# Performance work log

Hardware: AMD Instinct MI355X
Metric: run time of the kernel (lower is better)

The kernel has to match this reference:

```python
import jax, jax.numpy as jnp
import numpy as np

N, E, D, F = 8192, 262144, 256, 512  # nodes, edges, hidden_dim, ffn hidden
M = 256  # performer num_random_features (default)


def _ln(x, g, b, eps=1e-5):
    mu = jnp.mean(x, axis=-1, keepdims=True)
    var = jnp.mean((x - mu) ** 2, axis=-1, keepdims=True)
    return (x - mu) * jax.lax.rsqrt(var + eps) * g + b


def setup_inputs() -> dict:
    key = jax.random.key(0)
    ks = jax.random.split(key, 16)
    s = 1.0 / np.sqrt(D)
    return {
        "h": jax.random.normal(ks[0], (N, D), dtype=jnp.float32),
        "edge_index": jax.random.randint(ks[1], (2, E), 0, N, dtype=jnp.int32),
        "W_gcn": jax.random.normal(ks[2], (D, D), dtype=jnp.float32) * s,
        "b_gcn": jnp.zeros((D,), jnp.float32),
        "Wq": jax.random.normal(ks[3], (D, D), dtype=jnp.float32) * s,
        "bq": jnp.zeros((D,), jnp.float32),
        "Wk": jax.random.normal(ks[4], (D, D), dtype=jnp.float32) * s,
        "bk": jnp.zeros((D,), jnp.float32),
        "Wv": jax.random.normal(ks[5], (D, D), dtype=jnp.float32) * s,
        "bv": jnp.zeros((D,), jnp.float32),
        "Wo": jax.random.normal(ks[6], (D, D), dtype=jnp.float32) * s,
        "bo": jnp.zeros((D,), jnp.float32),
        "RF": jax.random.normal(ks[7], (M, D), dtype=jnp.float32) * s,  # random feature projection
        "g1": jnp.ones((D,), jnp.float32), "be1": jnp.zeros((D,), jnp.float32),
        "g2": jnp.ones((D,), jnp.float32), "be2": jnp.zeros((D,), jnp.float32),
        "g3": jnp.ones((D,), jnp.float32), "be3": jnp.zeros((D,), jnp.float32),
        "W1": jax.random.normal(ks[8], (D, F), dtype=jnp.float32) * s,
        "b1": jnp.zeros((F,), jnp.float32),
        "W2": jax.random.normal(ks[9], (F, D), dtype=jnp.float32) * (1.0 / np.sqrt(F)),
        "b2": jnp.zeros((D,), jnp.float32),
    }


def _gps_forward(h, edge_index, W_gcn, b_gcn, Wq, bq, Wk, bk, Wv, bv, Wo, bo, RF,
                 g1, be1, g2, be2, g3, be3, W1, b1, W2, b2):
    n = h.shape[0]
    # ---- local GCNConv (add self loops, symmetric norm) ----
    loops = jnp.arange(n, dtype=edge_index.dtype)
    src = jnp.concatenate([edge_index[0], loops])
    dst = jnp.concatenate([edge_index[1], loops])
    deg = jax.ops.segment_sum(jnp.ones_like(src, dtype=h.dtype), dst, num_segments=n)
    dinv = jnp.where(deg > 0, jax.lax.rsqrt(jnp.maximum(deg, 1e-12)), 0.0)
    coef = dinv[src] * dinv[dst]  # [E+N]
    xw = h @ W_gcn  # [N, D]
    h_local = jax.ops.segment_sum(xw[src] * coef[:, None], dst, num_segments=n) + b_gcn
    h1 = _ln(h + h_local, g1, be1)  # dropout p applied in train only; eval here
    # ---- global Performer attention (as written: dense NxN in feature space) ----
    q = h1 @ Wq + bq
    k = h1 @ Wk + bk
    v = h1 @ Wv + bv
    qf = q @ RF.T  # [N, M]
    kf = k @ RF.T  # [N, M]
    scores = (qf @ kf.T) / jnp.sqrt(jnp.asarray(h.shape[-1], h.dtype))  # [N, N]
    attw = jax.nn.softmax(scores, axis=-1)
    h_global = (attw @ v) @ Wo + bo
    h2 = _ln(h1 + h_global, g2, be2)
    # ---- FFN ----
    h_ffn = jnp.maximum(h2 @ W1 + b1, 0.0) @ W2 + b2
    return _ln(h2 + h_ffn, g3, be3)


def reference(h, edge_index, W_gcn, b_gcn, Wq, bq, Wk, bk, Wv, bv, Wo, bo, RF,
              g1, be1, g2, be2, g3, be3, W1, b1, W2, b2):
    return _gps_forward(h, edge_index, W_gcn, b_gcn, Wq, bq, Wk, bk, Wv, bv, Wo, bo, RF,
                        g1, be1, g2, be2, g3, be3, W1, b1, W2, b2)
```

## Files before the change

### kernel.cpp

```cpp
#include <hip/hip_runtime.h>
#include <hip/hip_bf16.h>

#define NN 8192
#define EE 262144
#define DD 256
#define FF 512
#define MM 256

typedef __attribute__((ext_vector_type(8))) short short8v;
typedef __attribute__((ext_vector_type(16))) float float16v;

__device__ __forceinline__ ushort f2bf(float x) {
  union { float f; unsigned u; } c; c.f = x;
  unsigned r = (c.u + 0x7FFF + ((c.u >> 16) & 1)) >> 16;
  return (ushort)r;
}
__device__ __forceinline__ float b2f(ushort u) {
  union { unsigned u; float f; } c; c.u = ((unsigned)u) << 16;
  return c.f;
}
__device__ __forceinline__ void async_copy16(void* lds, const void* g) {
  __builtin_amdgcn_global_load_lds(
      (const __attribute__((address_space(1))) void*)g,
      (__attribute__((address_space(3))) void*)lds, 16, 0, 0);
}

__global__ __launch_bounds__(1024) void scan_kernel(const int* __restrict__ degi,
                                                    int* __restrict__ csr_off,
                                                    float* __restrict__ dinv) {
  __shared__ int part[1024];
  int tid = threadIdx.x;
  int base = tid * 8;
  int loc[8], dv[8]; int s = 0;
#pragma unroll
  for (int i = 0; i < 8; ++i) { int d = degi[base + i]; dv[i] = d; loc[i] = s; s += d; }
  part[tid] = s;
  __syncthreads();
  for (int off = 1; off < 1024; off <<= 1) {
    int v = (tid >= off) ? part[tid - off] : 0;
    __syncthreads();
    part[tid] += v;
    __syncthreads();
  }
  int pre = (tid == 0) ? 0 : part[tid - 1];
#pragma unroll
  for (int i = 0; i < 8; ++i) {
    csr_off[base + i] = pre + loc[i];
    dinv[base + i] = rsqrtf((float)(dv[i] + 1));
  }
  if (tid == 1023) csr_off[NN] = part[1023];
}

__global__ void fill_kernel(const int* __restrict__ ei, const int* __restrict__ csr_off,
                            int* __restrict__ cursor, int* __restrict__ csr_src) {
  int i = blockIdx.x * blockDim.x + threadIdx.x;
  if (i < EE) {
    int d = ei[EE + i];
    int pos = csr_off[d] + atomicAdd(&cursor[d], 1);
    csr_src[pos] = ei[i];
  }
}

#define QSCALE 0.090168441f
#define P1B 10753
__global__ __launch_bounds__(256) void prep_kernel(
    const float* __restrict__ h, const float* __restrict__ W_gcn,
    const float* __restrict__ Wv, const float* __restrict__ Wo,
    const float* __restrict__ W1, const float* __restrict__ W2,
    const float* __restrict__ bv,
    const float* __restrict__ Wq, const float* __restrict__ Wk,
    const float* __restrict__ bq, const float* __restrict__ bk,
    const float* __restrict__ RF, const int* __restrict__ ei,
    ushort* __restrict__ hb, ushort* __restrict__ WgcnT, ushort* __restrict__ Wcat,
    ushort* __restrict__ WoT, ushort* __restrict__ W1T, ushort* __restrict__ W2T,
    ushort* __restrict__ RFb, ushort* __restrict__ Wqkb,
    float* __restrict__ bcat, int* __restrict__ degi)
{
  if (blockIdx.x < P1B) {
    int i = blockIdx.x * 256 + threadIdx.x;
    const int R0 = NN * DD;
    const int R1 = R0 + DD * DD;
    const int R2 = R1 + DD * DD;
    const int R3 = R2 + DD * DD;
    const int R4 = R3 + DD * FF;
    const int R5 = R4 + FF * DD;
    const int R6 = R5 + DD;
    const int R7 = R6 + DD * DD;
    const int R8 = R7 + DD * DD;
    const int R9 = R8 + DD * DD;
    if (i < R0) {
      hb[i] = f2bf(h[i]);
    } else if (i < R1) {
      int j = i - R0; int n = j >> 8, k = j & 255;
      WgcnT[(n << 8) | k] = f2bf(W_gcn[k * DD + n]);
    } else if (i < R2) {
      int j = i - R1; int n = j >> 8, k = j & 255;
      Wcat[((512 + n) << 8) | k] = f2bf(Wv[k * DD + n]);
    } else if (i < R3) {
      int j = i - R2; int n = j >> 8, k = j & 255;
      WoT[(n << 8) | k] = f2bf(Wo[k * DD + n]);
    } else if (i < R4) {
      int j = i - R3; int n = j >> 8, k = j & 255;
      W1T[(n << 8) | k] = f2bf(W1[k * FF + n]);
    } else if (i < R5) {
      int j = i - R4; int n = j >> 9, k = j & 511;
      W2T[n * FF + k] = f2bf(W2[k * DD + n]);
    } else if (i < R6) {
      bcat[512 + (i - R5)] = bv[i - R5];
    } else if (i < R7) {
      int j = i - R6;
      RFb[j] = f2bf(RF[j]);
    } else if (i < R8) {
      int j = i - R7;
      Wqkb[j] = f2bf(Wq[j] * QSCALE);
    } else if (i < R9) {
      int j = i - R8;
      Wqkb[DD * DD + j] = f2bf(Wk[j]);
    }
  } else if (blockIdx.x < P1B + 2) {
    const int b = blockIdx.x - P1B;
    const int m = threadIdx.x;
    const float* bvec = (b == 0) ? bq : bk;
    const float alpha = (b == 0) ? QSCALE : 1.0f;
    float s = 0.0f;
    for (int j = 0; j < DD; ++j) s = fmaf(bvec[j], RF[m * DD + j], s);
    bcat[(b == 0 ? 0 : 256) + m] = s * alpha;
  } else {
    int i = (blockIdx.x - P1B - 2) * 256 + threadIdx.x;
    if (i < EE) atomicAdd(&degi[ei[EE + i]], 1);
  }
}

template<int OMODE, bool RELU>
__global__ __launch_bounds__(512) void gemm_bf16_kernel(
    const ushort* __restrict__ A, const ushort* __restrict__ BT,
    const float* __restrict__ bias, void* __restrict__ Cv,
    void* __restrict__ Cv2, void* __restrict__ Cv3, void* __restrict__ Cv4,
    int M, int N, int K)
{
  __shared__ ushort As[2][4096];
  __shared__ ushort Bs[2][4096];
  const int tid = threadIdx.x;
  const int c32 = tid & 31, hi = (tid >> 5) & 1;
  const int wv = tid >> 6;
  const int q = wv & 3, ks = wv >> 2;
  const int qm = (q >> 1) << 5, qn = (q & 1) << 5;

  const ushort* pA = A;
  const ushort* pBT = BT;
  int m0 = blockIdx.y * 64;
  const int n0 = blockIdx.x * 64;
  bool xw_path = true;
  if (OMODE == 6) {
    if (blockIdx.y < 128) {
      if (blockIdx.x >= 4) return;
    } else {
      xw_path = false;
      pA = (const ushort*)Cv2;
      pBT = (const ushort*)Cv3;
      m0 = (blockIdx.y - 128) * 64;
    }
  }

  const int sr = tid >> 3, spsl = tid & 7;
  const int ssl = spsl ^ ((sr >> 2) & 7);
  const ushort* Asrc = pA + (size_t)(m0 + sr) * K + (ssl << 3);
  const ushort* Bsrc = pBT + (size_t)(n0 + sr) * K + (ssl << 3);

  const int ra = qm + c32, rb = qn + c32;
  const int ga = (ra >> 2) & 7, gb = (rb >> 2) & 7;

  float16v acc = (float16v)(0.0f);

#define GS(b, k0) { \
    async_copy16(&As[b][tid << 3], Asrc + (k0)); \
    async_copy16(&Bs[b][tid << 3], Bsrc + (k0)); }

  GS(0, 0)
  const int nk = K >> 6;
  for (int kt = 0; kt < nk; ++kt) {
    asm volatile("s_waitcnt vmcnt(0)" ::: "memory");
    __syncthreads();
    if (kt + 1 < nk) GS((kt + 1) & 1, (kt + 1) << 6)
    const ushort* as_ = As[kt & 1];
    const ushort* bs_ = Bs[kt & 1];
    __builtin_amdgcn_s_setprio(1);
#pragma unroll
    for (int k2 = 0; k2 < 2; ++k2) {
      const int k16 = (ks << 1) + k2;
      const int sl = (k16 << 1) + hi;
      short8v af = *(const short8v*)&as_[(ra << 6) + ((sl ^ ga) << 3)];
      short8v bf = *(const short8v*)&bs_[(rb << 6) + ((sl ^ gb) << 3)];
      acc = __builtin_amdgcn_mfma_f32_32x32x16_bf16(af, bf, acc, 0, 0, 0);
    }
    __builtin_amdgcn_s_setprio(0);
  }
#undef GS

  __syncthreads();
  float* red = (float*)&As[0][0];
  if (ks == 1) {
#pragma unroll
    for (int r = 0; r < 16; ++r) {
      const int crow = (r & 3) + ((r >> 2) << 3) + (hi << 2);
      red[(q << 10) + (crow << 5) + c32] = acc[r];
    }
  }
  __syncthreads();
  if (ks == 0) {
    const int col = n0 + qn + c32;
    const float bv = bias ? bias[col] : 0.0f;
    if (OMODE == 3 && col >= 512) {
#pragma unroll
      for (int g = 0; g < 4; ++g) {
        float v0 = acc[g * 4 + 0] + red[(q << 10) + (((0) + (g << 3) + (hi << 2)) << 5) + c32] + bv;
        float v1 = acc[g * 4 + 1] + red[(q << 10) + (((1) + (g << 3) + (hi << 2)) << 5) + c32] + bv;
        float v2 = acc[g * 4 + 2] + red[(q << 10) + (((2) + (g << 3) + (hi << 2)) << 5) + c32] + bv;
        float v3 = acc[g * 4 + 3] + red[(q << 10) + (((3) + (g << 3) + (hi << 2)) << 5) + c32] + bv;
        ushort4 o; o.x = f2bf(v0); o.y = f2bf(v1); o.z = f2bf(v2); o.w = f2bf(v3);
        *(ushort4*)&((ushort*)Cv3)[(size_t)(col - 512) * NN + m0 + qm + (g << 3) + (hi << 2)] = o;
      }
    } else {
#pragma unroll
      for (int r = 0; r < 16; ++r) {
        const int crow = (r & 3) + ((r >> 2) << 3) + (hi << 2);
        const int m = m0 + qm + crow;
        float v = acc[r] + red[(q << 10) + (crow << 5) + c32] + bv;
        if (RELU) v = fmaxf(v, 0.0f);
        if (OMODE == 4) {
          ((ushort*)Cv)[(size_t)m * N + col] = f2bf(v);
        } else if (OMODE == 6) {
          if (xw_path) {
            ((ushort*)Cv)[(size_t)m * 256 + col] = f2bf(v);
          } else {
            ushort* W = (ushort*)Cv4;
            if (col < 256) W[(size_t)m * 256 + col] = f2bf(v);
            else W[(size_t)(256 + m) * 256 + (col - 256)] = f2bf(v);
          }
        } else {
          if (col < 256) {
            ((ushort*)Cv)[(size_t)m * 256 + col] = f2bf(v);
          } else {
            const int c2 = (col - 256) ^ ((m & 7) << 3) ^ (((m >> 3) & 3) << 6);
            ((ushort*)Cv2)[(size_t)m * 256 + c2] = f2bf(v);
          }
        }
      }
    }
  }
}

__global__ __launch_bounds__(256) void gcn_gather_ln_kernel(
    const ushort* __restrict__ xwb, const float* __restrict__ h,
    const float* __restrict__ dinv, const int* __restrict__ csr_off,
    const int* __restrict__ csr_src, const float* __restrict__ b_gcn,
    const float* __restrict__ g1, const float* __restrict__ be1,
    ushort* __restrict__ h1b)
{
  const int node = blockIdx.x * 4 + (threadIdx.x >> 6);
  const int t = threadIdx.x & 63;
  const int c4 = t << 2;
  const float di = dinv[node];
  const int e0 = csr_off[node], e1 = csr_off[node + 1];
  float acc[4] = {0.f, 0.f, 0.f, 0.f};
  for (int e = e0; e < e1; ++e) {
    int s = csr_src[e];
    float ds = dinv[s];
    ushort4 xv = *(const ushort4*)&xwb[(size_t)s * DD + c4];
    acc[0] = fmaf(b2f(xv.x), ds, acc[0]);
    acc[1] = fmaf(b2f(xv.y), ds, acc[1]);
    acc[2] = fmaf(b2f(xv.z), ds, acc[2]);
    acc[3] = fmaf(b2f(xv.w), ds, acc[3]);
  }
  ushort4 sv = *(const ushort4*)&xwb[(size_t)node * DD + c4];
  float4 hv = *(const float4*)&h[(size_t)node * DD + c4];
  float4 bg = *(const float4*)&b_gcn[c4];
  const float dii = di * di;
  float y[4];
  y[0] = fmaf(acc[0], di, b2f(sv.x) * dii) + bg.x + hv.x;
  y[1] = fmaf(acc[1], di, b2f(sv.y) * dii) + bg.y + hv.y;
  y[2] = fmaf(acc[2], di, b2f(sv.z) * dii) + bg.z + hv.z;
  y[3] = fmaf(acc[3], di, b2f(sv.w) * dii) + bg.w + hv.w;
  float s1 = (y[0] + y[1]) + (y[2] + y[3]);
  float s2 = (y[0]*y[0] + y[1]*y[1]) + (y[2]*y[2] + y[3]*y[3]);
#pragma unroll
  for (int m = 1; m <= 32; m <<= 1) { s1 += __shfl_xor(s1, m); s2 += __shfl_xor(s2, m); }
  float mu = s1 * (1.0f / 256.0f);
  float var = s2 * (1.0f / 256.0f) - mu * mu;
  float inv = rsqrtf(fmaxf(var, 0.0f) + 1e-5f);
  float4 g4 = *(const float4*)&g1[c4];
  float4 b4 = *(const float4*)&be1[c4];
  float v0 = (y[0] - mu) * inv * g4.x + b4.x;
  float v1 = (y[1] - mu) * inv * g4.y + b4.y;
  float v2 = (y[2] - mu) * inv * g4.z + b4.z;
  float v3 = (y[3] - mu) * inv * g4.w + b4.w;
  ushort4 ob; ob.x = f2bf(v0); ob.y = f2bf(v1); ob.z = f2bf(v2); ob.w = f2bf(v3);
  *(ushort4*)&h1b[(node << 8) + c4] = ob;
}

__global__ __launch_bounds__(256, 2) void flash_mfma_kernel(
    const ushort* __restrict__ qb, const ushort* __restrict__ kb,
    const ushort* __restrict__ vbT, ushort* __restrict__ opb,
    float* __restrict__ ml, int ksn, int kchunk)
{
  __shared__ ushort Kbuf[2][8192];
  __shared__ ushort Vbuf[2][8192];

  const int tid = threadIdx.x;
  const int l = tid & 63, wv = tid >> 6;
  const int c32 = l & 31, hi = l >> 5;
  const int qt = blockIdx.x / ksn, ks = blockIdx.x % ksn;
  const int q0 = qt * 128;
  const int kbase = ks * kchunk;

  const int vrow = tid >> 2;
  const ushort* kptr = kb + (size_t)(kbase + (tid >> 5)) * 256 + ((tid & 31) << 3);
  const ushort* vptr = vbT + (size_t)vrow * NN + kbase + (((tid & 3) ^ ((vrow >> 3) & 3)) << 3);

#define FSTAGE(b) { \
    _Pragma("unroll") \
    for (int c = 0; c < 4; ++c) { \
      async_copy16(&Kbuf[b][((c << 8) + tid) << 3], kptr + (size_t)c * (8 * 256)); \
      async_copy16(&Vbuf[b][((c << 8) + tid) << 3], vptr + (size_t)c * (64 * NN)); \
    } }

  FSTAGE(0)

  short8v qfr[16];
  {
    const ushort* qrow = qb + (size_t)(q0 + wv * 32 + c32) * 256 + (hi << 3);
#pragma unroll
    for (int kk = 0; kk < 16; ++kk)
      qfr[kk] = *(const short8v*)(qrow + (kk << 4));
  }

  float16v acc[8];
#pragma unroll
  for (int dt = 0; dt < 8; ++dt) acc[dt] = (float16v)(0.0f);
  float lsum = 0.f;

  const int ksw = ((c32 & 7) << 3) | (((c32 >> 3) & 3) << 6);
  const int vsw = (c32 >> 3) & 3;
  const int voff0 = (hi ^ vsw) << 3;
  const int voff1 = ((2 + hi) ^ vsw) << 3;

  const int nit = kchunk >> 5;
  for (int it = 0; it < nit; ++it) {
    asm volatile("s_waitcnt vmcnt(0)" ::: "memory");
    __syncthreads();
    if (it + 1 < nit) {
      kptr += 32 * 256;
      vptr += 32;
      FSTAGE((it + 1) & 1)
    }
    const ushort* Kp = Kbuf[it & 1];
    const ushort* Vp = Vbuf[it & 1];

    float16v s = (float16v)(0.0f);
    __builtin_amdgcn_s_setprio(1);
#pragma unroll
    for (int kk = 0; kk < 16; ++kk) {
      short8v kf = *(const short8v*)&Kp[(c32 << 8) + (((kk << 4) + (hi << 3)) ^ ksw)];
      s = __builtin_amdgcn_mfma_f32_32x32x16_bf16(kf, qfr[kk], s, 0, 0, 0);
    }
    __builtin_amdgcn_s_setprio(0);

    float p[16];
#pragma unroll
    for (int r = 0; r < 16; ++r) p[r] = exp2f(s[r]);
    {
      float t0 = (p[0] + p[1]) + (p[2] + p[3]);
      float t1 = (p[4] + p[5]) + (p[6] + p[7]);
      float t2 = (p[8] + p[9]) + (p[10] + p[11]);
      float t3 = (p[12] + p[13]) + (p[14] + p[15]);
      lsum += (t0 + t1) + (t2 + t3);
    }
    unsigned u0, u1, u2, u3, u4, u5, u6, u7;
    asm("v_cvt_pk_bf16_f32 %0, %1, %2" : "=v"(u0) : "v"(p[0]),  "v"(p[1]));
    asm("v_cvt_pk_bf16_f32 %0, %1, %2" : "=v"(u1) : "v"(p[2]),  "v"(p[3]));
    asm("v_cvt_pk_bf16_f32 %0, %1, %2" : "=v"(u2) : "v"(p[4]),  "v"(p[5]));
    asm("v_cvt_pk_bf16_f32 %0, %1, %2" : "=v"(u3) : "v"(p[6]),  "v"(p[7]));
    asm("v_cvt_pk_bf16_f32 %0, %1, %2" : "=v"(u4) : "v"(p[8]),  "v"(p[9]));
    asm("v_cvt_pk_bf16_f32 %0, %1, %2" : "=v"(u5) : "v"(p[10]), "v"(p[11]));
    asm("v_cvt_pk_bf16_f32 %0, %1, %2" : "=v"(u6) : "v"(p[12]), "v"(p[13]));
    asm("v_cvt_pk_bf16_f32 %0, %1, %2" : "=v"(u7) : "v"(p[14]), "v"(p[15]));
    asm volatile("v_permlane32_swap_b32 %0, %1" : "+v"(u0), "+v"(u2));
    asm volatile("v_permlane32_swap_b32 %0, %1" : "+v"(u1), "+v"(u3));
    asm volatile("v_permlane32_swap_b32 %0, %1" : "+v"(u4), "+v"(u6));
    asm volatile("v_permlane32_swap_b32 %0, %1" : "+v"(u5), "+v"(u7));
    union { unsigned uu[4]; short8v v; } P0, P1;
    P0.uu[0] = u0; P0.uu[1] = u1; P0.uu[2] = u2; P0.uu[3] = u3;
    P1.uu[0] = u4; P1.uu[1] = u5; P1.uu[2] = u6; P1.uu[3] = u7;

    __builtin_amdgcn_s_setprio(1);
#pragma unroll
    for (int dt = 0; dt < 8; ++dt) {
      const int drow = (dt << 5) + c32;
      short8v vf0 = *(const short8v*)&Vp[(drow << 5) + voff0];
      short8v vf1 = *(const short8v*)&Vp[(drow << 5) + voff1];
      acc[dt] = __builtin_amdgcn_mfma_f32_32x32x16_bf16(P0.v, vf0, acc[dt], 0, 0, 0);
      acc[dt] = __builtin_amdgcn_mfma_f32_32x32x16_bf16(P1.v, vf1, acc[dt], 0, 0, 0);
    }
    __builtin_amdgcn_s_setprio(0);
  }
#undef FSTAGE

  float lt = lsum + __shfl_xor(lsum, 32);
  if (hi == 0) ml[(size_t)ks * NN + q0 + wv * 32 + c32] = lt;
  ushort* op = opb + (size_t)ks * (NN * DD);
#pragma unroll
  for (int dt = 0; dt < 8; ++dt)
#pragma unroll
    for (int r = 0; r < 16; ++r) {
      const int qrow = q0 + wv * 32 + (r & 3) + ((r >> 2) << 3) + (hi << 2);
      op[(size_t)qrow * DD + (dt << 5) + c32] = f2bf(acc[dt][r]);
    }
}

__global__ __launch_bounds__(512, 4) void epilogue_kernel(
    const ushort* __restrict__ opb, const float* __restrict__ ml,
    const ushort* __restrict__ h1b,
    const ushort* __restrict__ WoT, const float* __restrict__ bo,
    const float* __restrict__ g2, const float* __restrict__ be2,
    const ushort* __restrict__ W1T, const float* __restrict__ b1,
    const ushort* __restrict__ W2T, const float* __restrict__ b2,
    const float* __restrict__ g3, const float* __restrict__ be3,
    float* __restrict__ out, int ksn)
{
  __shared__ float  yL[32 * 256];
  __shared__ ushort h2bL[32 * 256];
  __shared__ ushort tL[32 * 512];

  ushort* hgL = tL;

  const int tid = threadIdx.x;
  const int c32 = tid & 31, hi = (tid >> 5) & 1;
  const int wv = tid >> 6;
  const int lane = tid & 63;
  const int m0 = blockIdx.x * 32;
  const int n0 = wv << 5;
  const int col = n0 + c32;

  {
    const int row = tid >> 4;
    const int cseg = (tid & 15) << 4;
    const int growp = m0 + row;
    float L = 0.f;
    for (int i = 0; i < ksn; ++i) L += ml[(size_t)i * NN + growp];
    const float invl = 1.0f / L;
    float num[16];
#pragma unroll
    for (int j = 0; j < 16; ++j) num[j] = 0.f;
    for (int i = 0; i < ksn; ++i) {
      const ushort* src = opb + (size_t)i * ((size_t)NN * DD) + (size_t)growp * DD + cseg;
      short8v v0 = *(const short8v*)src;
      short8v v1 = *(const short8v*)(src + 8);
#pragma unroll
      for (int j = 0; j < 8; ++j) {
        num[j]     += b2f((ushort)v0[j]);
        num[8 + j] += b2f((ushort)v1[j]);
      }
    }
    const int swz = (row & 7) ^ (((row >> 3) & 3) << 3);
    const int sl0 = (cseg >> 3);
    union { ushort us[8]; short8v v; } o0, o1;
#pragma unroll
    for (int j = 0; j < 8; ++j) {
      o0.us[j] = f2bf(num[j] * invl);
      o1.us[j] = f2bf(num[8 + j] * invl);
    }
    *(short8v*)&hgL[(row << 8) + ((sl0 ^ swz) << 3)] = o0.v;
    *(short8v*)&hgL[(row << 8) + (((sl0 + 1) ^ swz) << 3)] = o1.v;
  }
  __syncthreads();

  float16v acc = (float16v)(0.0f);
  {
    const int aswz = (c32 & 7) ^ (((c32 >> 3) & 3) << 3);
#pragma unroll
    for (int k0 = 0; k0 < 256; k0 += 16) {
      const int sA = (k0 >> 3) + hi;
      short8v af = *(const short8v*)&hgL[(c32 << 8) + ((sA ^ aswz) << 3)];
      short8v bf = *(const short8v*)&WoT[(size_t)col * 256 + k0 + (hi << 3)];
      acc = __builtin_amdgcn_mfma_f32_32x32x16_bf16(af, bf, acc, 0, 0, 0);
    }
  }
  {
    const float bov = bo[col];
#pragma unroll
    for (int r = 0; r < 16; ++r) {
      const int row = (r & 3) + ((r >> 2) << 3) + (hi << 2);
      yL[(row << 8) + col] = acc[r] + bov + b2f(h1b[(size_t)(m0 + row) * 256 + col]);
    }
  }
  __syncthreads();
#pragma unroll
  for (int rr = 0; rr < 4; ++rr) {
    const int row = (wv << 2) + rr;
    const int c4 = lane << 2;
    float4 v = *(const float4*)&yL[(row << 8) + c4];
    float s1 = (v.x + v.y) + (v.z + v.w);
    float s2 = (v.x * v.x + v.y * v.y) + (v.z * v.z + v.w * v.w);
#pragma unroll
    for (int m = 1; m <= 32; m <<= 1) { s1 += __shfl_xor(s1, m); s2 += __shfl_xor(s2, m); }
    float mu = s1 * (1.0f / 256.0f);
    float var = s2 * (1.0f / 256.0f) - mu * mu;
    float inv = rsqrtf(fmaxf(var, 0.0f) + 1e-5f);
    float4 g4 = *(const float4*)&g2[c4];
    float4 b4 = *(const float4*)&be2[c4];
    float o0 = (v.x - mu) * inv * g4.x + b4.x;
    float o1 = (v.y - mu) * inv * g4.y + b4.y;
    float o2 = (v.z - mu) * inv * g4.z + b4.z;
    float o3 = (v.w - mu) * inv * g4.w + b4.w;
    *(float4*)&yL[(row << 8) + c4] = make_float4(o0, o1, o2, o3);
    const int psl = (c4 >> 3) ^ (row & 7);
    ushort4 ob; ob.x = f2bf(o0); ob.y = f2bf(o1); ob.z = f2bf(o2); ob.w = f2bf(o3);
    *(ushort4*)&h2bL[(row << 8) + (psl << 3) + (c4 & 7)] = ob;
  }
  __syncthreads();
  {
    float16v a1[2] = {(float16v)(0.0f), (float16v)(0.0f)};
    const int f0 = wv << 6;
#pragma unroll
    for (int k0 = 0; k0 < 256; k0 += 16) {
      const int s = (k0 >> 3) + hi;
      short8v af = *(const short8v*)&h2bL[(c32 << 8) + ((s ^ (c32 & 7)) << 3)];
#pragma unroll
      for (int nt = 0; nt < 2; ++nt) {
        short8v bf = *(const short8v*)&W1T[(size_t)(f0 + (nt << 5) + c32) * 256 + k0 + (hi << 3)];
        a1[nt] = __builtin_amdgcn_mfma_f32_32x32x16_bf16(af, bf, a1[nt], 0, 0, 0);
      }
    }
#pragma unroll
    for (int nt = 0; nt < 2; ++nt) {
      const int col1 = f0 + (nt << 5) + c32;
      const float b1v = b1[col1];
#pragma unroll
      for (int r = 0; r < 16; ++r) {
        const int row = (r & 3) + ((r >> 2) << 3) + (hi << 2);
        float v = fmaxf(a1[nt][r] + b1v, 0.0f);
        const int psl = (col1 >> 3) ^ (row & 7);
        tL[(row << 9) + (psl << 3) + (col1 & 7)] = f2bf(v);
      }
    }
  }
  __syncthreads();
  float16v a2 = (float16v)(0.0f);
#pragma unroll
  for (int k0 = 0; k0 < 512; k0 += 16) {
    const int s = (k0 >> 3) + hi;
    short8v af = *(const short8v*)&tL[(c32 << 9) + ((s ^ (c32 & 7)) << 3)];
    short8v bf = *(const short8v*)&W2T[(size_t)col * 512 + k0 + (hi << 3)];
    a2 = __builtin_amdgcn_mfma_f32_32x32x16_bf16(af, bf, a2, 0, 0, 0);
  }
  {
    const float b2v = b2[col];
#pragma unroll
    for (int r = 0; r < 16; ++r) {
      const int row = (r & 3) + ((r >> 2) << 3) + (hi << 2);
      a2[r] += b2v + yL[(row << 8) + col];
    }
  }
  __syncthreads();
  {
    float* y2L = (float*)tL;
#pragma unroll
    for (int r = 0; r < 16; ++r) {
      const int row = (r & 3) + ((r >> 2) << 3) + (hi << 2);
      y2L[(row << 8) + col] = a2[r];
    }
  }
  __syncthreads();
  {
    const float* y2L = (const float*)tL;
#pragma unroll
    for (int rr = 0; rr < 4; ++rr) {
      const int row = (wv << 2) + rr;
      const int c4 = lane << 2;
      float4 v = *(const float4*)&y2L[(row << 8) + c4];
      float s1 = (v.x + v.y) + (v.z + v.w);
      float s2 = (v.x * v.x + v.y * v.y) + (v.z * v.z + v.w * v.w);
#pragma unroll
      for (int m = 1; m <= 32; m <<= 1) { s1 += __shfl_xor(s1, m); s2 += __shfl_xor(s2, m); }
      float mu = s1 * (1.0f / 256.0f);
      float var = s2 * (1.0f / 256.0f) - mu * mu;
      float inv = rsqrtf(fmaxf(var, 0.0f) + 1e-5f);
      float4 g4 = *(const float4*)&g3[c4];
      float4 b4 = *(const float4*)&be3[c4];
      float4 o;
      o.x = (v.x - mu) * inv * g4.x + b4.x;
      o.y = (v.y - mu) * inv * g4.y + b4.y;
      o.z = (v.z - mu) * inv * g4.z + b4.z;
      o.w = (v.w - mu) * inv * g4.w + b4.w;
      *(float4*)&out[(size_t)(m0 + row) * 256 + c4] = o;
    }
  }
}

extern "C" void kernel_launch(void* const* d_in, const int* in_sizes, int n_in,
                              void* d_out, int out_size, void* d_ws, size_t ws_size,
                              hipStream_t stream) {
  (void)in_sizes; (void)n_in; (void)out_size;
  const float* h     = (const float*)d_in[0];
  const int*   ei    = (const int*)  d_in[1];
  const float* W_gcn = (const float*)d_in[2];
  const float* b_gcn = (const float*)d_in[3];
  const float* Wq    = (const float*)d_in[4];
  const float* bq    = (const float*)d_in[5];
  const float* Wk    = (const float*)d_in[6];
  const float* bk    = (const float*)d_in[7];
  const float* Wv    = (const float*)d_in[8];
  const float* bv    = (const float*)d_in[9];
  const float* Wo    = (const float*)d_in[10];
  const float* bo    = (const float*)d_in[11];
  const float* RF    = (const float*)d_in[12];
  const float* g1    = (const float*)d_in[13];
  const float* be1   = (const float*)d_in[14];
  const float* g2    = (const float*)d_in[15];
  const float* be2   = (const float*)d_in[16];
  const float* g3    = (const float*)d_in[17];
  const float* be3   = (const float*)d_in[18];
  const float* W1    = (const float*)d_in[19];
  const float* b1    = (const float*)d_in[20];
  const float* W2    = (const float*)d_in[21];
  const float* b2    = (const float*)d_in[22];
  float* out = (float*)d_out;

  const size_t M2 = (size_t)NN * DD;
  const int ksn = (ws_size >= (size_t)64 * 1024 * 1024) ? 8 : 4;
  const int kchunk = NN / ksn;

  char* base = (char*)d_ws;
  ushort* hbX  = (ushort*)base; base += M2 * 2;
  ushort* h1bX = (ushort*)base; base += M2 * 2;
  ushort* qb   = (ushort*)base; base += M2 * 2;
  ushort* kb   = (ushort*)base; base += M2 * 2;
  ushort* vbT  = (ushort*)base; base += M2 * 2;
  ushort* opb  = (ushort*)base;
  float*  R    = (float*)opb;   base += (size_t)ksn * M2 * 2;
  float*  mlf  = (float*)base;  base += (size_t)8 * NN * 4;
  ushort* WgcnT = (ushort*)base; base += DD * DD * 2;
  ushort* Wcat  = (ushort*)base; base += (size_t)768 * DD * 2;
  ushort* WoT   = (ushort*)base; base += DD * DD * 2;
  ushort* W1T   = (ushort*)base; base += FF * DD * 2;
  ushort* W2T   = (ushort*)base; base += DD * FF * 2;
  ushort* RFb   = (ushort*)base; base += DD * DD * 2;
  ushort* Wqkb  = (ushort*)base; base += (size_t)2 * DD * DD * 2;
  float*  bcat  = (float*)base;  base += 768 * 4;
  float*  dinv  = (float*)base;  base += NN * 4;
  int* degi    = (int*)base; base += NN * 4;
  int* cursor  = (int*)base; base += NN * 4;
  int* csr_off = (int*)base; base += (NN + 4) * 4;
  int* csr_src = (int*)base; base += EE * 4;

  ushort* xwb = (ushort*)R;

  hipMemsetAsync(degi, 0, (size_t)2 * NN * sizeof(int), stream);

  prep_kernel<<<P1B + 2 + 1024, 256, 0, stream>>>(
      h, W_gcn, Wv, Wo, W1, W2, bv, Wq, Wk, bq, bk, RF, ei,
      hbX, WgcnT, Wcat, WoT, W1T, W2T, RFb, Wqkb, bcat, degi);

  gemm_bf16_kernel<6, false><<<dim3(8, 132), 512, 0, stream>>>(
      hbX, WgcnT, nullptr, xwb, RFb, Wqkb, Wcat, NN, DD, DD);

  scan_kernel<<<1, 1024, 0, stream>>>(degi, csr_off, dinv);
  fill_kernel<<<EE / 256, 256, 0, stream>>>(ei, csr_off, cursor, csr_src);

  gcn_gather_ln_kernel<<<NN / 4, 256, 0, stream>>>(xwb, h, dinv, csr_off, csr_src, b_gcn, g1, be1, h1bX);
  gemm_bf16_kernel<3, false><<<dim3(768 / 64, NN / 64), 512, 0, stream>>>(
      h1bX, Wcat, bcat, qb, kb, vbT, nullptr, NN, 768, DD);
  flash_mfma_kernel<<<(NN / 128) * ksn, 256, 0, stream>>>(qb, kb, vbT, opb, mlf, ksn, kchunk);
  epilogue_kernel<<<NN / 32, 512, 0, stream>>>(
      opb, mlf, h1bX, WoT, bo, g2, be2, W1T, b1, W2T, b2, g3, be3, out, ksn);
}
```

Measured before the change: 212.6 us.

## Load full-K A tile once and loop over multiple N tiles per block

The bf16 GEMM kernel now loads the whole 64x256 A tile (full K=256) into LDS once with an XOR swizzle. It then iterates over several 64-wide N tiles, loading each full-K B tile in turn. This removes the K-loop double buffering and the repeated A reloads across N-tile blocks, and launches far fewer blocks for the xw/RF and QKV projections. The cost is much more LDS per block (64KB for the tiles plus 16KB for the reduction) and serialized B loads, with only a partial overlap of the next B load against the epilogue.

```diff
diff --git a/kernel.cpp b/kernel.cpp
--- a/kernel.cpp
+++ b/kernel.cpp
@@ -132,14 +132,16 @@
 }
 
 template<int OMODE, bool RELU>
-__global__ __launch_bounds__(512) void gemm_bf16_kernel(
+__global__ __launch_bounds__(512, 2) void gemm_v3_kernel(
     const ushort* __restrict__ A, const ushort* __restrict__ BT,
     const float* __restrict__ bias, void* __restrict__ Cv,
     void* __restrict__ Cv2, void* __restrict__ Cv3, void* __restrict__ Cv4,
-    int M, int N, int K)
+    int NT)
 {
-  __shared__ ushort As[2][4096];
-  __shared__ ushort Bs[2][4096];
+  __shared__ ushort As[16384];
+  __shared__ ushort Bs[16384];
+  __shared__ float  red[4096];
+
   const int tid = threadIdx.x;
   const int c32 = tid & 31, hi = (tid >> 5) & 1;
   const int wv = tid >> 6;
@@ -149,105 +151,103 @@
   const ushort* pA = A;
   const ushort* pBT = BT;
   int m0 = blockIdx.y * 64;
-  const int n0 = blockIdx.x * 64;
+  int nt = NT;
   bool xw_path = true;
   if (OMODE == 6) {
-    if (blockIdx.y < 128) {
-      if (blockIdx.x >= 4) return;
-    } else {
+    if (blockIdx.y >= 128) {
       xw_path = false;
       pA = (const ushort*)Cv2;
       pBT = (const ushort*)Cv3;
       m0 = (blockIdx.y - 128) * 64;
-    }
-  }
-
-  const int sr = tid >> 3, spsl = tid & 7;
-  const int ssl = spsl ^ ((sr >> 2) & 7);
-  const ushort* Asrc = pA + (size_t)(m0 + sr) * K + (ssl << 3);
-  const ushort* Bsrc = pBT + (size_t)(n0 + sr) * K + (ssl << 3);
+      nt = 4;
+    }
+  }
+
+#pragma unroll
+  for (int i = 0; i < 4; ++i) {
+    int c = tid + (i << 9);
+    int row = c >> 5, psl = c & 31;
+    int ssl = psl ^ (row & 31);
+    async_copy16(&As[c << 3], &pA[(size_t)(m0 + row) * 256 + (ssl << 3)]);
+  }
+
+#define GSB(n0_) { \
+    _Pragma("unroll") \
+    for (int i = 0; i < 4; ++i) { \
+      int c = tid + (i << 9); \
+      int row = c >> 5, psl = c & 31; \
+      int ssl = psl ^ (row & 31); \
+      async_copy16(&Bs[c << 3], &pBT[(size_t)((n0_) + row) * 256 + (ssl << 3)]); \
+    } }
+
+  GSB((size_t)blockIdx.x * nt * 64)
 
   const int ra = qm + c32, rb = qn + c32;
-  const int ga = (ra >> 2) & 7, gb = (rb >> 2) & 7;
-
-  float16v acc = (float16v)(0.0f);
-
-#define GS(b, k0) { \
-    async_copy16(&As[b][tid << 3], Asrc + (k0)); \
-    async_copy16(&Bs[b][tid << 3], Bsrc + (k0)); }
-
-  GS(0, 0)
-  const int nk = K >> 6;
-  for (int kt = 0; kt < nk; ++kt) {
+  for (int j = 0; j < nt; ++j) {
+    const int n0 = (blockIdx.x * nt + j) * 64;
     asm volatile("s_waitcnt vmcnt(0)" ::: "memory");
     __syncthreads();
-    if (kt + 1 < nk) GS((kt + 1) & 1, (kt + 1) << 6)
-    const ushort* as_ = As[kt & 1];
-    const ushort* bs_ = Bs[kt & 1];
+    float16v acc = (float16v)(0.0f);
     __builtin_amdgcn_s_setprio(1);
 #pragma unroll
-    for (int k2 = 0; k2 < 2; ++k2) {
-      const int k16 = (ks << 1) + k2;
-      const int sl = (k16 << 1) + hi;
-      short8v af = *(const short8v*)&as_[(ra << 6) + ((sl ^ ga) << 3)];
-      short8v bf = *(const short8v*)&bs_[(rb << 6) + ((sl ^ gb) << 3)];
+    for (int kk = 0; kk < 8; ++kk) {
+      const int sl = (((ks << 3) + kk) << 1) + hi;
+      short8v af = *(const short8v*)&As[(ra << 8) + ((sl ^ c32) << 3)];
+      short8v bf = *(const short8v*)&Bs[(rb << 8) + ((sl ^ c32) << 3)];
       acc = __builtin_amdgcn_mfma_f32_32x32x16_bf16(af, bf, acc, 0, 0, 0);
     }
     __builtin_amdgcn_s_setprio(0);
-  }
-#undef GS
-
-  __syncthreads();
-  float* red = (float*)&As[0][0];
-  if (ks == 1) {
-#pragma unroll
-    for (int r = 0; r < 16; ++r) {
-      const int crow = (r & 3) + ((r >> 2) << 3) + (hi << 2);
-      red[(q << 10) + (crow << 5) + c32] = acc[r];
-    }
-  }
-  __syncthreads();
-  if (ks == 0) {
-    const int col = n0 + qn + c32;
-    const float bv = bias ? bias[col] : 0.0f;
-    if (OMODE == 3 && col >= 512) {
-#pragma unroll
-      for (int g = 0; g < 4; ++g) {
-        float v0 = acc[g * 4 + 0] + red[(q << 10) + (((0) + (g << 3) + (hi << 2)) << 5) + c32] + bv;
-        float v1 = acc[g * 4 + 1] + red[(q << 10) + (((1) + (g << 3) + (hi << 2)) << 5) + c32] + bv;
-        float v2 = acc[g * 4 + 2] + red[(q << 10) + (((2) + (g << 3) + (hi << 2)) << 5) + c32] + bv;
-        float v3 = acc[g * 4 + 3] + red[(q << 10) + (((3) + (g << 3) + (hi << 2)) << 5) + c32] + bv;
-        ushort4 o; o.x = f2bf(v0); o.y = f2bf(v1); o.z = f2bf(v2); o.w = f2bf(v3);
-        *(ushort4*)&((ushort*)Cv3)[(size_t)(col - 512) * NN + m0 + qm + (g << 3) + (hi << 2)] = o;
-      }
-    } else {
+    __syncthreads();
+    if (j + 1 < nt) GSB((size_t)(blockIdx.x * nt + j + 1) * 64)
+    if (ks == 1) {
 #pragma unroll
       for (int r = 0; r < 16; ++r) {
         const int crow = (r & 3) + ((r >> 2) << 3) + (hi << 2);
-        const int m = m0 + qm + crow;
-        float v = acc[r] + red[(q << 10) + (crow << 5) + c32] + bv;
-        if (RELU) v = fmaxf(v, 0.0f);
-        if (OMODE == 4) {
-          ((ushort*)Cv)[(size_t)m * N + col] = f2bf(v);
-        } else if (OMODE == 6) {
-          if (xw_path) {
-            ((ushort*)Cv)[(size_t)m * 256 + col] = f2bf(v);
+        red[(q << 10) + (crow << 5) + c32] = acc[r];
+      }
+    }
+    __syncthreads();
+    if (ks == 0) {
+      const int col = n0 + qn + c32;
+      const float bv = bias ? bias[col] : 0.0f;
+      if (OMODE == 3 && col >= 512) {
+#pragma unroll
+        for (int g = 0; g < 4; ++g) {
+          float v0 = acc[g * 4 + 0] + red[(q << 10) + (((0) + (g << 3) + (hi << 2)) << 5) + c32] + bv;
+          float v1 = acc[g * 4 + 1] + red[(q << 10) + (((1) + (g << 3) + (hi << 2)) << 5) + c32] + bv;
+          float v2 = acc[g * 4 + 2] + red[(q << 10) + (((2) + (g << 3) + (hi << 2)) << 5) + c32] + bv;
+          float v3 = acc[g * 4 + 3] + red[(q << 10) + (((3) + (g << 3) + (hi << 2)) << 5) + c32] + bv;
+          ushort4 o; o.x = f2bf(v0); o.y = f2bf(v1); o.z = f2bf(v2); o.w = f2bf(v3);
+          *(ushort4*)&((ushort*)Cv3)[(size_t)(col - 512) * NN + m0 + qm + (g << 3) + (hi << 2)] = o;
+        }
+      } else {
+#pragma unroll
+        for (int r = 0; r < 16; ++r) {
+          const int crow = (r & 3) + ((r >> 2) << 3) + (hi << 2);
+          const int m = m0 + qm + crow;
+          float v = acc[r] + red[(q << 10) + (crow << 5) + c32] + bv;
+          if (RELU) v = fmaxf(v, 0.0f);
+          if (OMODE == 6) {
+            if (xw_path) {
+              ((ushort*)Cv)[(size_t)m * 256 + col] = f2bf(v);
+            } else {
+              ushort* W = (ushort*)Cv4;
+              if (col < 256) W[(size_t)m * 256 + col] = f2bf(v);
+              else W[(size_t)(256 + m) * 256 + (col - 256)] = f2bf(v);
+            }
           } else {
-            ushort* W = (ushort*)Cv4;
-            if (col < 256) W[(size_t)m * 256 + col] = f2bf(v);
-            else W[(size_t)(256 + m) * 256 + (col - 256)] = f2bf(v);
-          }
-        } else {
-          if (col < 256) {
-            ((ushort*)Cv)[(size_t)m * 256 + col] = f2bf(v);
-          } else {
-            const int c2 = (col - 256) ^ ((m & 7) << 3) ^ (((m >> 3) & 3) << 6);
-            ((ushort*)Cv2)[(size_t)m * 256 + c2] = f2bf(v);
+            if (col < 256) {
+              ((ushort*)Cv)[(size_t)m * 256 + col] = f2bf(v);
+            } else {
+              const int c2 = (col - 256) ^ ((m & 7) << 3) ^ (((m >> 3) & 3) << 6);
+              ((ushort*)Cv2)[(size_t)m * 256 + c2] = f2bf(v);
+            }
           }
         }
       }
     }
   }
+#undef GSB
 }
 
 __global__ __launch_bounds__(256) void gcn_gather_ln_kernel(
@@ -661,15 +661,15 @@
       h, W_gcn, Wv, Wo, W1, W2, bv, Wq, Wk, bq, bk, RF, ei,
       hbX, WgcnT, Wcat, WoT, W1T, W2T, RFb, Wqkb, bcat, degi);
 
-  gemm_bf16_kernel<6, false><<<dim3(8, 132), 512, 0, stream>>>(
-      hbX, WgcnT, nullptr, xwb, RFb, Wqkb, Wcat, NN, DD, DD);
+  gemm_v3_kernel<6, false><<<dim3(2, 132), 512, 0, stream>>>(
+      hbX, WgcnT, nullptr, xwb, RFb, Wqkb, Wcat, 2);
 
   scan_kernel<<<1, 1024, 0, stream>>>(degi, csr_off, dinv);
   fill_kernel<<<EE / 256, 256, 0, stream>>>(ei, csr_off, cursor, csr_src);
 
   gcn_gather_ln_kernel<<<NN / 4, 256, 0, stream>>>(xwb, h, dinv, csr_off, csr_src, b_gcn, g1, be1, h1bX);
-  gemm_bf16_kernel<3, false><<<dim3(768 / 64, NN / 64), 512, 0, stream>>>(
-      h1bX, Wcat, bcat, qb, kb, vbT, nullptr, NN, 768, DD);
+  gemm_v3_kernel<3, false><<<dim3(4, 128), 512, 0, stream>>>(
+      h1bX, Wcat, bcat, qb, kb, vbT, nullptr, 3);
   flash_mfma_kernel<<<(NN / 128) * ksn, 256, 0, stream>>>(qb, kb, vbT, opb, mlf, ksn, kchunk);
   epilogue_kernel<<<NN / 32, 512, 0, stream>>>(
       opb, mlf, h1bX, WoT, bo, g2, be2, W1T, b1, W2T, b2, g3, be3, out, ksn);
```

Result: no change. 214.6 us (+0.9%).
